# Performance work log

Hardware: AMD Instinct MI355X
Metric: run time of the kernel (lower is better)

## Reference

```python
import jax, jax.numpy as jnp
import numpy as np

NUM_HEADS = 4
NUM_GROUPS = 32
EPS = 1e-5

def setup_inputs() -> dict:
    key = jax.random.key(0)
    ks = jax.random.split(key, 3)
    B, C, H, W = 4, 256, 64, 64
    x = jax.random.normal(ks[0], (B, C, H, W), jnp.float32)
    gn_w = jnp.ones((C,), jnp.float32)
    gn_b = jnp.zeros((C,), jnp.float32)
    qkv_w = jax.random.normal(ks[1], (3 * C, C), jnp.float32) * 0.02
    qkv_b = jnp.zeros((3 * C,), jnp.float32)
    proj_w = jax.random.normal(ks[2], (C, C), jnp.float32) * 0.02
    proj_b = jnp.zeros((C,), jnp.float32)
    return dict(x=x, gn_w=gn_w, gn_b=gn_b, qkv_w=qkv_w, qkv_b=qkv_b,
                proj_w=proj_w, proj_b=proj_b)

def reference(x, gn_w, gn_b, qkv_w, qkv_b, proj_w, proj_b):
    B, C, H, W = x.shape
    n = H * W
    xf = x.reshape(B, C, n)
    # GroupNorm(32, C) over (channels-in-group, n)
    xg = xf.reshape(B, NUM_GROUPS, -1)
    mu = xg.mean(-1, keepdims=True)
    var = xg.var(-1, keepdims=True)
    xn = ((xg - mu) * jax.lax.rsqrt(var + EPS)).reshape(B, C, n)
    xn = xn * gn_w[None, :, None] + gn_b[None, :, None]
    # 1x1 conv QKV: [B, 3C, n]
    qkv = jnp.einsum('oc,bcn->bon', qkv_w, xn) + qkv_b[None, :, None]
    # head split exactly as torch: reshape(B*heads, 3C//heads, n) then chunk
    qkv = qkv.reshape(B * NUM_HEADS, 3 * C // NUM_HEADS, n)
    q, k, v = jnp.split(qkv, 3, axis=1)  # each [B*heads, head_dim, n]
    scale = (C // NUM_HEADS) ** -0.25
    w = jnp.einsum('bct,bcs->bts', q * scale, k * scale)  # [B*heads, n, n]
    w = jax.nn.softmax(w, axis=-1)
    h = jnp.einsum('bts,bcs->bct', w, v).reshape(B, C, n)
    h = jnp.einsum('oc,bcn->bon', proj_w, h) + proj_b[None, :, None]
    return x + h.reshape(B, C, H, W)
```

## Files before the change

### kernel.cpp

```cpp
#include <hip/hip_runtime.h>

typedef unsigned short u16;
typedef unsigned int u32;
typedef __bf16 bf16x8 __attribute__((ext_vector_type(8)));
typedef float f32x4 __attribute__((ext_vector_type(4)));
typedef u16 u16x4 __attribute__((ext_vector_type(4)));
typedef u16 u16x8 __attribute__((ext_vector_type(8)));

#define MFMA16x16x32(a, b, c) __builtin_amdgcn_mfma_f32_16x16x32_bf16((a), (b), (c), 0, 0, 0)

static constexpr int kB = 4;
static constexpr int kC = 256;
static constexpr int kN = 4096;
static constexpr int kHeads = 4;
static constexpr int kD = 64;
static constexpr float kScale = 0.35355339059327373f;
static constexpr float kScaleQ = 0.51006971545f;

__device__ __forceinline__ u16 f2bf(float f) {
  union { float f; u32 i; } v; v.f = f;
  return (u16)((v.i + 0x7fffu + ((v.i >> 16) & 1u)) >> 16);
}
__device__ __forceinline__ bf16x8 ldb8(const u16* p) {
  return *reinterpret_cast<const bf16x8*>(p);
}
__device__ __forceinline__ float fast_exp2(float x) {
#if __has_builtin(__builtin_amdgcn_exp2f)
  return __builtin_amdgcn_exp2f(x);
#else
  float r;
  asm("v_exp_f32 %0, %1" : "=v"(r) : "v"(x));
  return r;
#endif
}

__global__ void convert_bf16_2(const float* __restrict__ in1, u16* __restrict__ out1,
                               int n1, const float* __restrict__ in2,
                               u16* __restrict__ out2, int n2) {
  const int total = n1 + n2;
  for (int i = blockIdx.x * blockDim.x + threadIdx.x; i < total;
       i += gridDim.x * blockDim.x) {
    if (i < n1) out1[i] = f2bf(in1[i]);
    else out2[i - n1] = f2bf(in2[i - n1]);
  }
}

__global__ __launch_bounds__(1024) void gn_kernel(const float* __restrict__ x,
                                                  const float* __restrict__ gnw,
                                                  const float* __restrict__ gnb,
                                                  u16* __restrict__ xnT) {
  const int g = blockIdx.x, b = blockIdx.y;
  const int tid = threadIdx.x;
  const float* xb = x + b * (kC * kN) + g * 8 * kN;
  float vals[4][8];
  float s = 0.f, ss = 0.f;
#pragma unroll
  for (int kk = 0; kk < 4; ++kk) {
    const int t = tid + kk * 1024;
#pragma unroll
    for (int c = 0; c < 8; ++c) {
      const float v_ = xb[c * kN + t];
      vals[kk][c] = v_;
      s += v_; ss += v_ * v_;
    }
  }
#pragma unroll
  for (int off = 32; off > 0; off >>= 1) {
    s += __shfl_down(s, off);
    ss += __shfl_down(ss, off);
  }
  __shared__ float rbuf[32];
  const int wid = tid >> 6, lane = tid & 63;
  if (lane == 0) { rbuf[wid] = s; rbuf[16 + wid] = ss; }
  __syncthreads();
  if (tid < 64) {
    float s2 = (lane < 16) ? rbuf[lane] : 0.f;
    float ss2 = (lane < 16) ? rbuf[16 + lane] : 0.f;
#pragma unroll
    for (int off = 8; off > 0; off >>= 1) {
      s2 += __shfl_down(s2, off);
      ss2 += __shfl_down(ss2, off);
    }
    if (lane == 0) { rbuf[0] = s2; rbuf[1] = ss2; }
  }
  __syncthreads();
  const float inv_n = 1.f / 32768.f;
  const float mu = rbuf[0] * inv_n;
  const float var = rbuf[1] * inv_n - mu * mu;
  const float rs = rsqrtf(var + 1e-5f);
  float wv[8], bv[8];
#pragma unroll
  for (int c = 0; c < 8; ++c) {
    const float wgt = gnw[g * 8 + c] * rs;
    wv[c] = wgt;
    bv[c] = gnb[g * 8 + c] - mu * wgt;
  }
  u16* ob = xnT + b * (kN * kC) + g * 8;
#pragma unroll
  for (int kk = 0; kk < 4; ++kk) {
    const int t = tid + kk * 1024;
    u16x8 pk;
#pragma unroll
    for (int c = 0; c < 8; ++c) pk[c] = f2bf(vals[kk][c] * wv[c] + bv[c]);
    *reinterpret_cast<u16x8*>(ob + t * kC) = pk;
  }
}

__global__ __launch_bounds__(256) void qkv_gemm(const u16* __restrict__ qkvw,
                                                const float* __restrict__ qkvb,
                                                const u16* __restrict__ xnT,
                                                u16* __restrict__ qt,
                                                u16* __restrict__ kt,
                                                u16* __restrict__ vv) {
  const int nblk = blockIdx.x, mblk = blockIdx.y, b = blockIdx.z;
  const int tid = threadIdx.x;
  const int w = tid >> 6, l = tid & 63, quad = l >> 4, col = l & 15;
  const int m0 = mblk * 64 + w * 16;
  const int n0 = nblk * 64;
  __shared__ __align__(16) u16 als[64 * 256];
  __shared__ __align__(16) u16 bls[64 * 256];
  {
    const u16* asrc = qkvw + (size_t)(mblk * 64) * kC;
    const u16* bsrc = xnT + (size_t)b * (kN * kC) + (size_t)n0 * kC;
#pragma unroll
    for (int p = 0; p < 8; ++p) {
      const int li = p * 256 + tid;
      const int row = li >> 5, ch = li & 31;
      const int sw = (ch ^ (row & 7)) * 8;
      *reinterpret_cast<bf16x8*>(&als[row * 256 + sw]) = ldb8(asrc + li * 8);
      *reinterpret_cast<bf16x8*>(&bls[row * 256 + sw]) = ldb8(bsrc + li * 8);
    }
  }
  __syncthreads();
  f32x4 acc[4] = {{0,0,0,0},{0,0,0,0},{0,0,0,0},{0,0,0,0}};
  const u16* arow = &als[(w * 16 + col) * 256];
  const int kx = col & 7;
#pragma unroll
  for (int ks = 0; ks < 8; ++ks) {
    const bf16x8 af = ldb8(arow + (((ks * 4 + quad) ^ kx)) * 8);
#pragma unroll
    for (int nt = 0; nt < 4; ++nt) {
      const bf16x8 bfr =
          ldb8(&bls[(nt * 16 + col) * 256 + (((ks * 4 + quad) ^ kx)) * 8]);
      acc[nt] = MFMA16x16x32(af, bfr, acc[nt]);
    }
  }
  const int o_base = m0 + quad * 4;
  const int head = o_base / 192;
  const int rr = o_base % 192;
  const int bh = b * kHeads + head;
  const int seg = rr >> 6;
  const int c0 = rr & 63;
  float bias[4];
#pragma unroll
  for (int r = 0; r < 4; ++r) bias[r] = qkvb[o_base + r];
  const float sc = (seg == 0) ? kScaleQ : kScale;
#pragma unroll
  for (int nt = 0; nt < 4; ++nt) {
    const int t = n0 + nt * 16 + col;
    if (seg == 2) {
      const int tp = n0 + (nt >> 1) * 32 + 8 * (col >> 2) + 4 * (nt & 1) + (col & 3);
#pragma unroll
      for (int r = 0; r < 4; ++r)
        vv[bh * (kD * kN) + (c0 + r) * kN + tp] = f2bf(acc[nt][r] + bias[r]);
    } else {
      u16* dst = (seg == 0 ? qt : kt) + bh * (kN * kD) + t * kD + c0;
      u16x4 pk;
#pragma unroll
      for (int r = 0; r < 4; ++r) pk[r] = f2bf((acc[nt][r] + bias[r]) * sc);
      *reinterpret_cast<u16x4*>(dst) = pk;
    }
  }
}

__global__ __launch_bounds__(256, 4) void attn_split(const u16* __restrict__ qt,
                                                     const u16* __restrict__ kt,
                                                     const u16* __restrict__ vv,
                                                     u16* __restrict__ ht) {
  const int tblk = blockIdx.x, bh = blockIdx.y;
  const int tid = threadIdx.x;
  const int w = tid >> 6, l = tid & 63, quad = l >> 4, col = l & 15;
  const int t0 = tblk * 128 + w * 32;
  const u16* qb = qt + bh * (kN * kD);
  const u16* kb = kt + bh * (kN * kD);
  const u16* vb = vv + bh * (kD * kN);
  bf16x8 qf[2][2];
#pragma unroll
  for (int ti = 0; ti < 2; ++ti) {
    qf[ti][0] = ldb8(qb + (t0 + ti * 16 + col) * kD + quad * 8);
    qf[ti][1] = ldb8(qb + (t0 + ti * 16 + col) * kD + 32 + quad * 8);
  }
  u16x8 ones_u;
#pragma unroll
  for (int i = 0; i < 8; ++i) ones_u[i] = 0x3f80;
  const bf16x8 onesf = *reinterpret_cast<bf16x8*>(&ones_u);
  f32x4 oacc[2][4];
  f32x4 lacc[2];
#pragma unroll
  for (int ti = 0; ti < 2; ++ti) {
    lacc[ti] = f32x4{0, 0, 0, 0};
#pragma unroll
    for (int ct = 0; ct < 4; ++ct) oacc[ti][ct] = f32x4{0, 0, 0, 0};
  }

  __shared__ __align__(16) u16 kls[2][2][32][64];
  __shared__ __align__(16) u16 vls[2][2][32][64];
  constexpr int NIT = kN / 64;

  const int srow = tid >> 3, sk8 = tid & 7, skey = srow & 7;
  const u16* ksrc = kb + (size_t)srow * kD + sk8 * 8;
  u16* kdst = &kls[0][0][srow][((sk8 ^ skey)) * 8];
  const int sa = sk8 >> 2, sq = sk8 & 3;
  const u16* vsrc = vb + (size_t)(2 * srow + sa) * kN + sq * 8;
  u16* vdst = &vls[0][0][srow][(((sa << 2) | sq) ^ skey) * 8];

  bf16x8 kstg0 = ldb8(ksrc);
  bf16x8 kstg1 = ldb8(ksrc + 32 * kD);
  bf16x8 vstg0 = ldb8(vsrc);
  bf16x8 vstg1 = ldb8(vsrc + 32);

#pragma unroll 2
  for (int it = 0; it < NIT; ++it) {
    const int cb = (it & 1) * (2 * 32 * 64);
    *reinterpret_cast<bf16x8*>(kdst + cb) = kstg0;
    *reinterpret_cast<bf16x8*>(kdst + cb + 2048) = kstg1;
    *reinterpret_cast<bf16x8*>(vdst + cb) = vstg0;
    *reinterpret_cast<bf16x8*>(vdst + cb + 2048) = vstg1;
    __syncthreads();
    if (it + 1 < NIT) {
      const size_t sb = (size_t)(it + 1) * 64;
      kstg0 = ldb8(ksrc + sb * kD);
      kstg1 = ldb8(ksrc + (sb + 32) * kD);
      vstg0 = ldb8(vsrc + sb);
      vstg1 = ldb8(vsrc + sb + 32);
    }
    const int kx = (col & 7) * 8;
    const int vslot = (((col & 1) << 2) | quad) ^ (col >> 1);
#pragma unroll
    for (int h = 0; h < 2; ++h) {
      const u16* kl = &kls[0][0][0][0] + cb + h * 2048;
      const u16* vl = &vls[0][0][0][0] + cb + h * 2048;
      const bf16x8 k00 = ldb8(kl + col * 64 + ((quad * 8) ^ kx));
      const bf16x8 k01 = ldb8(kl + col * 64 + ((32 + quad * 8) ^ kx));
      const bf16x8 k10 = ldb8(kl + (col + 16) * 64 + ((quad * 8) ^ kx));
      const bf16x8 k11 = ldb8(kl + (col + 16) * 64 + ((32 + quad * 8) ^ kx));
      bf16x8 vf[4];
#pragma unroll
      for (int ct = 0; ct < 4; ++ct)
        vf[ct] = ldb8(vl + (ct * 8 + (col >> 1)) * 64 + vslot * 8);
#pragma unroll
      for (int ti = 0; ti < 2; ++ti) {
        f32x4 sa0 = {0, 0, 0, 0}, sa1 = {0, 0, 0, 0};
        sa0 = MFMA16x16x32(k00, qf[ti][0], sa0);
        sa0 = MFMA16x16x32(k01, qf[ti][1], sa0);
        sa1 = MFMA16x16x32(k10, qf[ti][0], sa1);
        sa1 = MFMA16x16x32(k11, qf[ti][1], sa1);
        const u32 e00 = __float_as_uint(fast_exp2(sa0[0]));
        const u32 e01 = __float_as_uint(fast_exp2(sa0[1]));
        const u32 e02 = __float_as_uint(fast_exp2(sa0[2]));
        const u32 e03 = __float_as_uint(fast_exp2(sa0[3]));
        const u32 e10 = __float_as_uint(fast_exp2(sa1[0]));
        const u32 e11 = __float_as_uint(fast_exp2(sa1[1]));
        const u32 e12 = __float_as_uint(fast_exp2(sa1[2]));
        const u32 e13 = __float_as_uint(fast_exp2(sa1[3]));
        union { u32 wd[4]; bf16x8 v; } pa;
        pa.wd[0] = __builtin_amdgcn_perm(e01, e00, 0x07060302u);
        pa.wd[1] = __builtin_amdgcn_perm(e03, e02, 0x07060302u);
        pa.wd[2] = __builtin_amdgcn_perm(e11, e10, 0x07060302u);
        pa.wd[3] = __builtin_amdgcn_perm(e13, e12, 0x07060302u);
#pragma unroll
        for (int ct = 0; ct < 4; ++ct)
          oacc[ti][ct] = MFMA16x16x32(pa.v, vf[ct], oacc[ti][ct]);
        lacc[ti] = MFMA16x16x32(pa.v, onesf, lacc[ti]);
      }
    }
  }
  const int b = bh >> 2, head = bh & 3;
  u16* hb = ht + (size_t)b * (kN * kC) + head * kD;
#pragma unroll
  for (int ti = 0; ti < 2; ++ti)
#pragma unroll
    for (int r = 0; r < 4; ++r) {
      const int t = t0 + ti * 16 + quad * 4 + r;
      const float inv = 1.f / lacc[ti][r];
#pragma unroll
      for (int ct = 0; ct < 4; ++ct)
        hb[(size_t)t * kC + ct * 16 + col] = f2bf(oacc[ti][ct][r] * inv);
    }
}

__global__ __launch_bounds__(256) void proj_kernel(const u16* __restrict__ projw,
                                                   const float* __restrict__ projb,
                                                   const u16* __restrict__ ht,
                                                   const float* __restrict__ x,
                                                   float* __restrict__ out) {
  const int nblk = blockIdx.x, mblk = blockIdx.y, b = blockIdx.z;
  const int tid = threadIdx.x;
  const int w = tid >> 6, l = tid & 63, quad = l >> 4, col = l & 15;
  const int m0 = mblk * 64 + w * 16;
  const int n0 = nblk * 64;
  __shared__ __align__(16) u16 als[64 * 256];
  __shared__ __align__(16) u16 bls[64 * 256];
  {
    const u16* asrc = projw + (size_t)(mblk * 64) * kC;
    const u16* bsrc = ht + (size_t)b * (kN * kC) + (size_t)n0 * kC;
#pragma unroll
    for (int p = 0; p < 8; ++p) {
      const int li = p * 256 + tid;
      const int row = li >> 5, ch = li & 31;
      const int sw = (ch ^ (row & 7)) * 8;
      *reinterpret_cast<bf16x8*>(&als[row * 256 + sw]) = ldb8(asrc + li * 8);
      *reinterpret_cast<bf16x8*>(&bls[row * 256 + sw]) = ldb8(bsrc + li * 8);
    }
  }
  __syncthreads();
  f32x4 acc[4] = {{0,0,0,0},{0,0,0,0},{0,0,0,0},{0,0,0,0}};
  const u16* arow = &als[(w * 16 + col) * 256];
  const int kx = col & 7;
#pragma unroll
  for (int ks = 0; ks < 8; ++ks) {
    const bf16x8 af = ldb8(arow + (((ks * 4 + quad) ^ kx)) * 8);
#pragma unroll
    for (int nt = 0; nt < 4; ++nt) {
      const bf16x8 bfr =
          ldb8(&bls[(nt * 16 + col) * 256 + (((ks * 4 + quad) ^ kx)) * 8]);
      acc[nt] = MFMA16x16x32(af, bfr, acc[nt]);
    }
  }
#pragma unroll
  for (int nt = 0; nt < 4; ++nt) {
    const int t = n0 + nt * 16 + col;
#pragma unroll
    for (int r = 0; r < 4; ++r) {
      const int o = m0 + quad * 4 + r;
      const int idx = b * (kC * kN) + o * kN + t;
      out[idx] = acc[nt][r] + projb[o] + x[idx];
    }
  }
}

extern "C" void kernel_launch(void* const* d_in, const int* in_sizes, int n_in,
                              void* d_out, int out_size, void* d_ws, size_t ws_size,
                              hipStream_t stream) {
  const float* x = (const float*)d_in[0];
  const float* gnw = (const float*)d_in[1];
  const float* gnb = (const float*)d_in[2];
  const float* qkvw_f = (const float*)d_in[3];
  const float* qkvb = (const float*)d_in[4];
  const float* projw_f = (const float*)d_in[5];
  const float* projb = (const float*)d_in[6];
  float* out = (float*)d_out;

  char* ws = (char*)d_ws;
  u16* xnT = (u16*)(ws);
  u16* qt = (u16*)(ws + (8u << 20));
  u16* kt = (u16*)(ws + (16u << 20));
  u16* vv = (u16*)(ws + (24u << 20));
  u16* ht = (u16*)(ws + (32u << 20));
  u16* qkvw = (u16*)(ws + (40u << 20));
  u16* projw = (u16*)(ws + (41u << 20));

  convert_bf16_2<<<dim3(256), dim3(256), 0, stream>>>(qkvw_f, qkvw, 768 * kC,
                                                      projw_f, projw, kC * kC);
  gn_kernel<<<dim3(32, 4), dim3(1024), 0, stream>>>(x, gnw, gnb, xnT);
  qkv_gemm<<<dim3(64, 12, 4), dim3(256), 0, stream>>>(qkvw, qkvb, xnT, qt, kt, vv);
  attn_split<<<dim3(32, 16), dim3(256), 0, stream>>>(qt, kt, vv, ht);
  proj_kernel<<<dim3(64, 4, 4), dim3(256), 0, stream>>>(projw, projb, ht, x, out);
}
```

Measured before the change: 192.1 us.

## Split attention work across 8 waves with 16 query rows each

The attention kernel now launches 512 threads per block instead of 256, and each wave handles 16 query rows instead of 32. K/V tile staging is spread across twice as many threads, so each thread loads one 16-byte chunk of K and V per iteration instead of two. The goal is more waves in flight to hide the exp and LDS latency, with fewer registers per wave. The cost is that each K/V fragment read from LDS feeds half as many MFMAs, so LDS read traffic per FLOP doubles and the per-iteration barriers cover more waves.

```diff
diff --git a/kernel.cpp b/kernel.cpp
--- a/kernel.cpp
+++ b/kernel.cpp
@@ -173,66 +173,53 @@
   }
 }
 
-__global__ __launch_bounds__(256, 4) void attn_split(const u16* __restrict__ qt,
+__global__ __launch_bounds__(512, 4) void attn_split(const u16* __restrict__ qt,
                                                      const u16* __restrict__ kt,
                                                      const u16* __restrict__ vv,
                                                      u16* __restrict__ ht) {
   const int tblk = blockIdx.x, bh = blockIdx.y;
   const int tid = threadIdx.x;
   const int w = tid >> 6, l = tid & 63, quad = l >> 4, col = l & 15;
-  const int t0 = tblk * 128 + w * 32;
+  const int t0 = tblk * 128 + w * 16;
   const u16* qb = qt + bh * (kN * kD);
   const u16* kb = kt + bh * (kN * kD);
   const u16* vb = vv + bh * (kD * kN);
-  bf16x8 qf[2][2];
-#pragma unroll
-  for (int ti = 0; ti < 2; ++ti) {
-    qf[ti][0] = ldb8(qb + (t0 + ti * 16 + col) * kD + quad * 8);
-    qf[ti][1] = ldb8(qb + (t0 + ti * 16 + col) * kD + 32 + quad * 8);
-  }
+  bf16x8 qf0, qf1;
+  qf0 = ldb8(qb + (t0 + col) * kD + quad * 8);
+  qf1 = ldb8(qb + (t0 + col) * kD + 32 + quad * 8);
   u16x8 ones_u;
 #pragma unroll
   for (int i = 0; i < 8; ++i) ones_u[i] = 0x3f80;
   const bf16x8 onesf = *reinterpret_cast<bf16x8*>(&ones_u);
-  f32x4 oacc[2][4];
-  f32x4 lacc[2];
-#pragma unroll
-  for (int ti = 0; ti < 2; ++ti) {
-    lacc[ti] = f32x4{0, 0, 0, 0};
-#pragma unroll
-    for (int ct = 0; ct < 4; ++ct) oacc[ti][ct] = f32x4{0, 0, 0, 0};
-  }
+  f32x4 oacc[4];
+  f32x4 lacc = {0, 0, 0, 0};
+#pragma unroll
+  for (int ct = 0; ct < 4; ++ct) oacc[ct] = f32x4{0, 0, 0, 0};
 
   __shared__ __align__(16) u16 kls[2][2][32][64];
   __shared__ __align__(16) u16 vls[2][2][32][64];
   constexpr int NIT = kN / 64;
 
-  const int srow = tid >> 3, sk8 = tid & 7, skey = srow & 7;
-  const u16* ksrc = kb + (size_t)srow * kD + sk8 * 8;
-  u16* kdst = &kls[0][0][srow][((sk8 ^ skey)) * 8];
-  const int sa = sk8 >> 2, sq = sk8 & 3;
-  const u16* vsrc = vb + (size_t)(2 * srow + sa) * kN + sq * 8;
-  u16* vdst = &vls[0][0][srow][(((sa << 2) | sq) ^ skey) * 8];
-
-  bf16x8 kstg0 = ldb8(ksrc);
-  bf16x8 kstg1 = ldb8(ksrc + 32 * kD);
-  bf16x8 vstg0 = ldb8(vsrc);
-  bf16x8 vstg1 = ldb8(vsrc + 32);
+  const int r6 = tid >> 3, c3 = tid & 7;
+  const u16* ksrc = kb + (size_t)r6 * kD + c3 * 8;
+  u16* kdst = &kls[0][r6 >> 5][r6 & 31][(c3 ^ (r6 & 7)) * 8];
+  const int vh = r6 >> 5, vr = r6 & 31, sa = c3 >> 2, sq = c3 & 3;
+  const u16* vsrc = vb + (size_t)(2 * vr + sa) * kN + vh * 32 + sq * 8;
+  u16* vdst = &vls[0][vh][vr][(((sa << 2) | sq) ^ (vr & 7)) * 8];
+
+  bf16x8 kstg = ldb8(ksrc);
+  bf16x8 vstg = ldb8(vsrc);
 
 #pragma unroll 2
   for (int it = 0; it < NIT; ++it) {
     const int cb = (it & 1) * (2 * 32 * 64);
-    *reinterpret_cast<bf16x8*>(kdst + cb) = kstg0;
-    *reinterpret_cast<bf16x8*>(kdst + cb + 2048) = kstg1;
-    *reinterpret_cast<bf16x8*>(vdst + cb) = vstg0;
-    *reinterpret_cast<bf16x8*>(vdst + cb + 2048) = vstg1;
+    *reinterpret_cast<bf16x8*>(kdst + cb) = kstg;
+    *reinterpret_cast<bf16x8*>(vdst + cb) = vstg;
     __syncthreads();
     if (it + 1 < NIT) {
       const size_t sb = (size_t)(it + 1) * 64;
-      kstg0 = ldb8(ksrc + sb * kD);
-      kstg1 = ldb8(ksrc + (sb + 32) * kD);
-      vstg0 = ldb8(vsrc + sb);
-      vstg1 = ldb8(vsrc + sb + 32);
+      kstg = ldb8(ksrc + sb * kD);
+      vstg = ldb8(vsrc + sb);
     }
     const int kx = (col & 7) * 8;
     const int vslot = (((col & 1) << 2) | quad) ^ (col >> 1);
@@ -248,45 +235,40 @@
 #pragma unroll
       for (int ct = 0; ct < 4; ++ct)
         vf[ct] = ldb8(vl + (ct * 8 + (col >> 1)) * 64 + vslot * 8);
-#pragma unroll
-      for (int ti = 0; ti < 2; ++ti) {
-        f32x4 sa0 = {0, 0, 0, 0}, sa1 = {0, 0, 0, 0};
-        sa0 = MFMA16x16x32(k00, qf[ti][0], sa0);
-        sa0 = MFMA16x16x32(k01, qf[ti][1], sa0);
-        sa1 = MFMA16x16x32(k10, qf[ti][0], sa1);
-        sa1 = MFMA16x16x32(k11, qf[ti][1], sa1);
-        const u32 e00 = __float_as_uint(fast_exp2(sa0[0]));
-        const u32 e01 = __float_as_uint(fast_exp2(sa0[1]));
-        const u32 e02 = __float_as_uint(fast_exp2(sa0[2]));
-        const u32 e03 = __float_as_uint(fast_exp2(sa0[3]));
-        const u32 e10 = __float_as_uint(fast_exp2(sa1[0]));
-        const u32 e11 = __float_as_uint(fast_exp2(sa1[1]));
-        const u32 e12 = __float_as_uint(fast_exp2(sa1[2]));
-        const u32 e13 = __float_as_uint(fast_exp2(sa1[3]));
-        union { u32 wd[4]; bf16x8 v; } pa;
-        pa.wd[0] = __builtin_amdgcn_perm(e01, e00, 0x07060302u);
-        pa.wd[1] = __builtin_amdgcn_perm(e03, e02, 0x07060302u);
-        pa.wd[2] = __builtin_amdgcn_perm(e11, e10, 0x07060302u);
-        pa.wd[3] = __builtin_amdgcn_perm(e13, e12, 0x07060302u);
-#pragma unroll
-        for (int ct = 0; ct < 4; ++ct)
-          oacc[ti][ct] = MFMA16x16x32(pa.v, vf[ct], oacc[ti][ct]);
-        lacc[ti] = MFMA16x16x32(pa.v, onesf, lacc[ti]);
-      }
+      f32x4 sa0 = {0, 0, 0, 0}, sa1 = {0, 0, 0, 0};
+      sa0 = MFMA16x16x32(k00, qf0, sa0);
+      sa0 = MFMA16x16x32(k01, qf1, sa0);
+      sa1 = MFMA16x16x32(k10, qf0, sa1);
+      sa1 = MFMA16x16x32(k11, qf1, sa1);
+      const u32 e00 = __float_as_uint(fast_exp2(sa0[0]));
+      const u32 e01 = __float_as_uint(fast_exp2(sa0[1]));
+      const u32 e02 = __float_as_uint(fast_exp2(sa0[2]));
+      const u32 e03 = __float_as_uint(fast_exp2(sa0[3]));
+      const u32 e10 = __float_as_uint(fast_exp2(sa1[0]));
+      const u32 e11 = __float_as_uint(fast_exp2(sa1[1]));
+      const u32 e12 = __float_as_uint(fast_exp2(sa1[2]));
+      const u32 e13 = __float_as_uint(fast_exp2(sa1[3]));
+      union { u32 wd[4]; bf16x8 v; } pa;
+      pa.wd[0] = __builtin_amdgcn_perm(e01, e00, 0x07060302u);
+      pa.wd[1] = __builtin_amdgcn_perm(e03, e02, 0x07060302u);
+      pa.wd[2] = __builtin_amdgcn_perm(e11, e10, 0x07060302u);
+      pa.wd[3] = __builtin_amdgcn_perm(e13, e12, 0x07060302u);
+#pragma unroll
+      for (int ct = 0; ct < 4; ++ct)
+        oacc[ct] = MFMA16x16x32(pa.v, vf[ct], oacc[ct]);
+      lacc = MFMA16x16x32(pa.v, onesf, lacc);
     }
   }
   const int b = bh >> 2, head = bh & 3;
   u16* hb = ht + (size_t)b * (kN * kC) + head * kD;
 #pragma unroll
-  for (int ti = 0; ti < 2; ++ti)
-#pragma unroll
-    for (int r = 0; r < 4; ++r) {
-      const int t = t0 + ti * 16 + quad * 4 + r;
-      const float inv = 1.f / lacc[ti][r];
-#pragma unroll
-      for (int ct = 0; ct < 4; ++ct)
-        hb[(size_t)t * kC + ct * 16 + col] = f2bf(oacc[ti][ct][r] * inv);
-    }
+  for (int r = 0; r < 4; ++r) {
+    const int t = t0 + quad * 4 + r;
+    const float inv = 1.f / lacc[r];
+#pragma unroll
+    for (int ct = 0; ct < 4; ++ct)
+      hb[(size_t)t * kC + ct * 16 + col] = f2bf(oacc[ct][r] * inv);
+  }
 }
 
 __global__ __launch_bounds__(256) void proj_kernel(const u16* __restrict__ projw,
@@ -364,6 +346,6 @@
                                                       projw_f, projw, kC * kC);
   gn_kernel<<<dim3(32, 4), dim3(1024), 0, stream>>>(x, gnw, gnb, xnT);
   qkv_gemm<<<dim3(64, 12, 4), dim3(256), 0, stream>>>(qkvw, qkvb, xnT, qt, kt, vv);
-  attn_split<<<dim3(32, 16), dim3(256), 0, stream>>>(qt, kt, vv, ht);
+  attn_split<<<dim3(32, 16), dim3(512), 0, stream>>>(qt, kt, vv, ht);
   proj_kernel<<<dim3(64, 4, 4), dim3(256), 0, stream>>>(projw, projb, ht, x, out);
 }
```

Result: no change. 192.5 us (+0.2%).
